# Performance work log

Measured on AMD Instinct MI355X. Metric: run time of the kernel, lower is better.

The kernel has to match this reference:

```python
import jax, jax.numpy as jnp
import numpy as np

IMAGE_SIZE = 256
BATCH = 128
CHANNELS = 3
NUM_STEPS = 32


def dct_matrix(N, dtype=jnp.float32):
    """Orthonormal DCT-II matrix D such that dct(x, norm='ortho') = D @ x."""
    n = jnp.arange(N, dtype=dtype)
    k = n[:, None]
    D = jnp.sqrt(2.0 / N) * jnp.cos(jnp.pi * (n[None, :] + 0.5) * k / N)
    return D.at[0].multiply(1.0 / jnp.sqrt(2.0))


def setup_inputs() -> dict:
    key = jax.random.key(0)
    k1, k2 = jax.random.split(key)
    x = jax.random.normal(k1, (BATCH, CHANNELS, IMAGE_SIZE, IMAGE_SIZE), dtype=jnp.float32)
    # geometric-ish blur schedule sigma in (0, 16]
    blur_sigmas = 0.5 * jnp.arange(1, NUM_STEPS + 1, dtype=jnp.float32)
    fwd_steps = jax.random.randint(k2, (BATCH,), 0, NUM_STEPS)
    return {"x": x, "blur_sigmas": blur_sigmas, "fwd_steps": fwd_steps}


def reference(x, blur_sigmas, fwd_steps):
    N = x.shape[-1]
    D = dct_matrix(N, x.dtype)
    # frequency grid: freqs[k] = pi * k / N
    freqs = jnp.pi * jnp.arange(N, dtype=x.dtype) / N
    freq_sq = freqs[:, None] ** 2 + freqs[None, :] ** 2  # [H, W]
    sigmas = blur_sigmas[fwd_steps][:, None, None, None]  # [B,1,1,1]
    t = sigmas ** 2 / 2.0
    # 2D DCT (ortho): apply D along H and W -> two GEMMs
    coefs = jnp.einsum('hi,bcij,wj->bchw', D, x, D)
    # elementwise spectral heat decay
    coefs = coefs * jnp.exp(-freq_sq * t)
    # 2D inverse DCT (ortho) = transpose transforms
    return jnp.einsum('ih,bchw,jw->bcij', D, coefs, D)
```

## Files before the change

### kernel.cpp

```cpp
#include <hip/hip_runtime.h>
#include <hip/hip_bf16.h>


#define NN 256
#define NSTEP 32

typedef __attribute__((ext_vector_type(8))) __bf16 bf16x8;
typedef __attribute__((ext_vector_type(4))) float f32x4;
typedef __attribute__((ext_vector_type(8))) unsigned short u16x8;
typedef __attribute__((ext_vector_type(4))) unsigned short u16x4;

__device__ __align__(16) float g_D[NN][NN];
__device__ __align__(16) unsigned short g_H[NSTEP][NN][NN];

static __device__ inline unsigned short f2bfu(float x) {
  unsigned u = __builtin_bit_cast(unsigned, x);
  u += 0x7fffu + ((u >> 16) & 1u);
  return (unsigned short)(u >> 16);
}

__global__ void compute_D() {
  int k = blockIdx.x;
  int n = threadIdx.x;
  int q = (k * (2 * n + 1)) & 1023;
  float c = cosf((float)q * (float)(M_PI / 512.0));
  float v = 0.08838834764831845f * c;
  if (k == 0) v *= 0.70710678118654752f;
  g_D[k][n] = v;
}

__global__ void compute_H(const float* __restrict__ sigmas) {
  __shared__ float a[8][NN];
  int s = blockIdx.x >> 5;
  int i0 = (blockIdx.x & 31) * 8;
  int j = threadIdx.x;

  float sg = sigmas[s];
  float t = 0.5f * sg * sg;
  float fk = (float)M_PI * (float)j * (1.0f / (float)NN);
  float m = expf(-fk * fk * t);
#pragma unroll
  for (int r = 0; r < 8; ++r) a[r][j] = g_D[i0 + r][j] * m;
  __syncthreads();

  float acc[8];
#pragma unroll
  for (int r = 0; r < 8; ++r) acc[r] = 0.f;
  for (int k = 0; k < NN; ++k) {
    float d = g_D[k][j];
#pragma unroll
    for (int r = 0; r < 8; ++r) acc[r] += a[r][k] * d;
  }
#pragma unroll
  for (int r = 0; r < 8; ++r) g_H[s][i0 + r][j] = f2bfu(acc[r]);
}

__global__ __launch_bounds__(512, 2) void dct_blur_main(
    const float* __restrict__ x, const int* __restrict__ steps,
    float* __restrict__ out) {
  __shared__ __align__(16) unsigned short Zt[128 * 256];

  int bid = blockIdx.x;
  int img = bid >> 1;
  int half = bid & 1;
  int b = img / 3;
  int s = steps[b];

  const float* X = x + (size_t)img * (NN * NN);
  float* O = out + (size_t)img * (NN * NN);
  const unsigned short* H = &g_H[s][0][0];

  int tid = (int)threadIdx.x;
  int lane = tid & 63;
  int w = tid >> 6;
  int wr = w >> 1;
  int wc = w & 1;
  int l16 = lane & 15;
  int hi = lane >> 4;

  int j0 = half * 128;
  int mrow0 = wr * 64;
  int ncol0 = wc * 64;

  f32x4 acc[4][4];
#pragma unroll
  for (int mi = 0; mi < 4; ++mi)
#pragma unroll
    for (int ni = 0; ni < 4; ++ni)
      acc[mi][ni] = (f32x4){0.f, 0.f, 0.f, 0.f};

#pragma unroll 2
  for (int kk = 0; kk < 8; ++kk) {
    int m0 = kk * 32;
    bf16x8 a[4], bb[4];
#pragma unroll
    for (int mi = 0; mi < 4; ++mi) {
      int row = mrow0 + mi * 16 + l16;
      const f32x4* p = reinterpret_cast<const f32x4*>(X + row * NN + m0 + hi * 8);
      f32x4 v0 = p[0], v1 = p[1];
      u16x8 r;
#pragma unroll
      for (int e = 0; e < 4; ++e) { r[e] = f2bfu(v0[e]); r[4 + e] = f2bfu(v1[e]); }
      a[mi] = __builtin_bit_cast(bf16x8, r);
    }
#pragma unroll
    for (int ni = 0; ni < 4; ++ni) {
      int hrow = j0 + ncol0 + ni * 16 + l16;
      u16x8 g = *reinterpret_cast<const u16x8*>(H + hrow * NN + m0 + hi * 8);
      bb[ni] = __builtin_bit_cast(bf16x8, g);
    }
#pragma unroll
    for (int mi = 0; mi < 4; ++mi)
#pragma unroll
      for (int ni = 0; ni < 4; ++ni)
        acc[mi][ni] = __builtin_amdgcn_mfma_f32_16x16x32_bf16(a[mi], bb[ni], acc[mi][ni], 0, 0, 0);
  }

#pragma unroll
  for (int mi = 0; mi < 4; ++mi) {
#pragma unroll
    for (int ni = 0; ni < 4; ++ni) {
      int j = ncol0 + ni * 16 + l16;
      int kb = mrow0 + mi * 16 + 4 * hi;
      u16x4 pk;
#pragma unroll
      for (int r = 0; r < 4; ++r) pk[r] = f2bfu(acc[mi][ni][r]);
      int idx = ((j << 8) + kb) ^ ((j & 7) << 3);
      *reinterpret_cast<u16x4*>(&Zt[idx]) = pk;
    }
  }

  __syncthreads();

  f32x4 acc2[4][4];
#pragma unroll
  for (int mi = 0; mi < 4; ++mi)
#pragma unroll
    for (int ni = 0; ni < 4; ++ni)
      acc2[mi][ni] = (f32x4){0.f, 0.f, 0.f, 0.f};

#pragma unroll 2
  for (int kk = 0; kk < 8; ++kk) {
    int k0 = kk * 32;
    bf16x8 a2[4], b2[4];
#pragma unroll
    for (int mi = 0; mi < 4; ++mi) {
      int irow = mrow0 + mi * 16 + l16;
      u16x8 g = *reinterpret_cast<const u16x8*>(H + irow * NN + k0 + hi * 8);
      a2[mi] = __builtin_bit_cast(bf16x8, g);
    }
#pragma unroll
    for (int ni = 0; ni < 4; ++ni) {
      int jr = ncol0 + ni * 16 + l16;
      int idx = ((jr << 8) + k0 + hi * 8) ^ ((jr & 7) << 3);
      u16x8 z = *reinterpret_cast<const u16x8*>(&Zt[idx]);
      b2[ni] = __builtin_bit_cast(bf16x8, z);
    }
#pragma unroll
    for (int mi = 0; mi < 4; ++mi)
#pragma unroll
      for (int ni = 0; ni < 4; ++ni)
        acc2[mi][ni] = __builtin_amdgcn_mfma_f32_16x16x32_bf16(a2[mi], b2[ni], acc2[mi][ni], 0, 0, 0);
  }

#pragma unroll
  for (int mi = 0; mi < 4; ++mi) {
#pragma unroll
    for (int ni = 0; ni < 4; ++ni) {
      int ibase = mrow0 + mi * 16 + 4 * hi;
      int jg = j0 + ncol0 + ni * 16 + l16;
#pragma unroll
      for (int r = 0; r < 4; ++r)
        O[(ibase + r) * NN + jg] = acc2[mi][ni][r];
    }
  }
}

extern "C" void kernel_launch(void* const* d_in, const int* in_sizes, int n_in,
                              void* d_out, int out_size, void* d_ws, size_t ws_size,
                              hipStream_t stream) {
  (void)in_sizes; (void)n_in; (void)out_size; (void)d_ws; (void)ws_size;
  const float* x = (const float*)d_in[0];
  const float* sigmas = (const float*)d_in[1];
  const int* steps = (const int*)d_in[2];
  float* out = (float*)d_out;

  compute_D<<<dim3(NN), dim3(NN), 0, stream>>>();
  compute_H<<<dim3(NSTEP * 32), dim3(NN), 0, stream>>>(sigmas);
  dct_blur_main<<<dim3(768), dim3(512), 0, stream>>>(x, steps, out);
}
```

Baseline: 282.2 us.

## Build H via trig-sum closed form and split main GEMMs into two global passes

The precompute is replaced: instead of building the DCT matrix and doing a 256^3 matmul per step, H is derived from per-step cosine/sine sums (compute_U) using a recurrence for the Gaussian weights, then assembled elementwise. The fused main kernel is split into two kernels that pass the intermediate bf16 product through a global scratch buffer, using 256-thread blocks over image quadrants with an XCD-aware block remap. This is meant to cut precompute cost and raise occupancy, at the price of an extra global round-trip for the intermediate and reduced precision in the H construction.

```diff
diff --git a/kernel.cpp b/kernel.cpp
--- a/kernel.cpp
+++ b/kernel.cpp
@@ -1,17 +1,22 @@
 #include <hip/hip_runtime.h>
 #include <hip/hip_bf16.h>
+#include <math.h>
 
 
 #define NN 256
 #define NSTEP 32
+#define NIMG 384
 
 typedef __attribute__((ext_vector_type(8))) __bf16 bf16x8;
+typedef __attribute__((ext_vector_type(4))) __bf16 bf16x4;
 typedef __attribute__((ext_vector_type(4))) float f32x4;
 typedef __attribute__((ext_vector_type(8))) unsigned short u16x8;
 typedef __attribute__((ext_vector_type(4))) unsigned short u16x4;
 
-__device__ __align__(16) float g_D[NN][NN];
+__device__ __align__(16) float g_Uc[NSTEP][512];
+__device__ __align__(16) float g_Us[NSTEP][512];
 __device__ __align__(16) unsigned short g_H[NSTEP][NN][NN];
+__device__ __align__(16) unsigned short g_PT[NIMG * NN * NN];
 
 static __device__ inline unsigned short f2bfu(float x) {
   unsigned u = __builtin_bit_cast(unsigned, x);
@@ -19,68 +24,66 @@
   return (unsigned short)(u >> 16);
 }
 
-__global__ void compute_D() {
-  int k = blockIdx.x;
-  int n = threadIdx.x;
-  int q = (k * (2 * n + 1)) & 1023;
-  float c = cosf((float)q * (float)(M_PI / 512.0));
-  float v = 0.08838834764831845f * c;
-  if (k == 0) v *= 0.70710678118654752f;
-  g_D[k][n] = v;
-}
-
-__global__ void compute_H(const float* __restrict__ sigmas) {
-  __shared__ float a[8][NN];
-  int s = blockIdx.x >> 5;
-  int i0 = (blockIdx.x & 31) * 8;
-  int j = threadIdx.x;
-
+__global__ void compute_U(const float* __restrict__ sigmas) {
+  int s = blockIdx.x >> 3;
+  int q = ((blockIdx.x & 7) << 6) + threadIdx.x;
+  int p = 2 * q + 1;
   float sg = sigmas[s];
   float t = 0.5f * sg * sg;
-  float fk = (float)M_PI * (float)j * (1.0f / (float)NN);
-  float m = expf(-fk * fk * t);
-#pragma unroll
-  for (int r = 0; r < 8; ++r) a[r][j] = g_D[i0 + r][j] * m;
-  __syncthreads();
-
-  float acc[8];
-#pragma unroll
-  for (int r = 0; r < 8; ++r) acc[r] = 0.f;
-  for (int k = 0; k < NN; ++k) {
-    float d = g_D[k][j];
-#pragma unroll
-    for (int r = 0; r < 8; ++r) acc[r] += a[r][k] * d;
-  }
-#pragma unroll
-  for (int r = 0; r < 8; ++r) g_H[s][i0 + r][j] = f2bfu(acc[r]);
-}
-
-__global__ __launch_bounds__(512, 2) void dct_blur_main(
-    const float* __restrict__ x, const int* __restrict__ steps,
-    float* __restrict__ out) {
-  __shared__ __align__(16) unsigned short Zt[128 * 256];
-
+  float c = (float)(M_PI / 256.0) * (float)(M_PI / 256.0) * t;
+  float m = __expf(-c);
+  float ratio = __expf(-3.0f * c);
+  float qf = __expf(-2.0f * c);
+  float sumc = 0.70710678118654752f;
+  float sums = 0.0f;
+  for (int k = 1; k < NN; ++k) {
+    int ph = (k * p) & 1023;
+    float ang = (float)ph * (float)(M_PI / 512.0);
+    float sn, cs;
+    sincosf(ang, &sn, &cs);
+    sumc += m * cs;
+    sums += m * sn;
+    m *= ratio;
+    ratio *= qf;
+  }
+  g_Uc[s][q] = sumc;
+  g_Us[s][q] = sums;
+}
+
+__global__ void compute_H(const float* __restrict__ sigmas) {
+  int s = blockIdx.x >> 8;
+  int i = blockIdx.x & 255;
+  int j = threadIdx.x;
+  int q1 = ((2 * (i - j) - 1) & 1023) >> 1;
+  int q2 = ((2 * (i + j) + 1) & 1023) >> 1;
+  float phi = (float)i * (float)(M_PI / 512.0);
+  float sp, cp;
+  sincosf(phi, &sp, &cp);
+  float v = (g_Uc[s][q1] + g_Uc[s][q2]) * cp - (g_Us[s][q1] + g_Us[s][q2]) * sp;
+  v *= (1.0f / (float)NN);
+  if (i == 0) v *= 0.70710678118654752f;
+  g_H[s][i][j] = f2bfu(v);
+}
+
+__global__ __launch_bounds__(256, 3) void dct_pass1(
+    const float* __restrict__ x, const int* __restrict__ steps) {
   int bid = blockIdx.x;
-  int img = bid >> 1;
-  int half = bid & 1;
-  int b = img / 3;
-  int s = steps[b];
+  int task = (bid & 7) * 192 + (bid >> 3);
+  int img = task >> 2;
+  int quad = task & 3;
+  int s = steps[img / 3];
 
   const float* X = x + (size_t)img * (NN * NN);
-  float* O = out + (size_t)img * (NN * NN);
   const unsigned short* H = &g_H[s][0][0];
+  unsigned short* PT = g_PT + (size_t)img * (NN * NN);
 
   int tid = (int)threadIdx.x;
   int lane = tid & 63;
   int w = tid >> 6;
-  int wr = w >> 1;
-  int wc = w & 1;
   int l16 = lane & 15;
   int hi = lane >> 4;
-
-  int j0 = half * 128;
-  int mrow0 = wr * 64;
-  int ncol0 = wc * 64;
+  int mrow0 = (quad >> 1) * 128 + (w >> 1) * 64;
+  int ncol0 = (quad & 1) * 128 + (w & 1) * 64;
 
   f32x4 acc[4][4];
 #pragma unroll
@@ -94,20 +97,20 @@
     int m0 = kk * 32;
     bf16x8 a[4], bb[4];
 #pragma unroll
+    for (int ni = 0; ni < 4; ++ni) {
+      int hrow = ncol0 + ni * 16 + l16;
+      u16x8 g = *reinterpret_cast<const u16x8*>(H + hrow * NN + m0 + hi * 8);
+      bb[ni] = __builtin_bit_cast(bf16x8, g);
+    }
+#pragma unroll
     for (int mi = 0; mi < 4; ++mi) {
       int row = mrow0 + mi * 16 + l16;
       const f32x4* p = reinterpret_cast<const f32x4*>(X + row * NN + m0 + hi * 8);
       f32x4 v0 = p[0], v1 = p[1];
-      u16x8 r;
-#pragma unroll
-      for (int e = 0; e < 4; ++e) { r[e] = f2bfu(v0[e]); r[4 + e] = f2bfu(v1[e]); }
-      a[mi] = __builtin_bit_cast(bf16x8, r);
-    }
-#pragma unroll
-    for (int ni = 0; ni < 4; ++ni) {
-      int hrow = j0 + ncol0 + ni * 16 + l16;
-      u16x8 g = *reinterpret_cast<const u16x8*>(H + hrow * NN + m0 + hi * 8);
-      bb[ni] = __builtin_bit_cast(bf16x8, g);
+      bf16x8 av;
+#pragma unroll
+      for (int e = 0; e < 4; ++e) { av[e] = (__bf16)v0[e]; av[4 + e] = (__bf16)v1[e]; }
+      a[mi] = av;
     }
 #pragma unroll
     for (int mi = 0; mi < 4; ++mi)
@@ -121,46 +124,63 @@
 #pragma unroll
     for (int ni = 0; ni < 4; ++ni) {
       int j = ncol0 + ni * 16 + l16;
-      int kb = mrow0 + mi * 16 + 4 * hi;
-      u16x4 pk;
-#pragma unroll
-      for (int r = 0; r < 4; ++r) pk[r] = f2bfu(acc[mi][ni][r]);
-      int idx = ((j << 8) + kb) ^ ((j & 7) << 3);
-      *reinterpret_cast<u16x4*>(&Zt[idx]) = pk;
-    }
-  }
-
-  __syncthreads();
-
-  f32x4 acc2[4][4];
+      int rb = mrow0 + mi * 16 + 4 * hi;
+      bf16x4 pk;
+#pragma unroll
+      for (int r = 0; r < 4; ++r) pk[r] = (__bf16)acc[mi][ni][r];
+      *reinterpret_cast<u16x4*>(PT + j * NN + rb) = __builtin_bit_cast(u16x4, pk);
+    }
+  }
+}
+
+__global__ __launch_bounds__(256, 3) void dct_pass2(
+    const int* __restrict__ steps, float* __restrict__ out) {
+  int bid = blockIdx.x;
+  int task = (bid & 7) * 192 + (bid >> 3);
+  int img = task >> 2;
+  int quad = task & 3;
+  int s = steps[img / 3];
+
+  const unsigned short* H = &g_H[s][0][0];
+  const unsigned short* PT = g_PT + (size_t)img * (NN * NN);
+  float* O = out + (size_t)img * (NN * NN);
+
+  int tid = (int)threadIdx.x;
+  int lane = tid & 63;
+  int w = tid >> 6;
+  int l16 = lane & 15;
+  int hi = lane >> 4;
+  int mrow0 = (quad >> 1) * 128 + (w >> 1) * 64;
+  int ncol0 = (quad & 1) * 128 + (w & 1) * 64;
+
+  f32x4 acc[4][4];
 #pragma unroll
   for (int mi = 0; mi < 4; ++mi)
 #pragma unroll
     for (int ni = 0; ni < 4; ++ni)
-      acc2[mi][ni] = (f32x4){0.f, 0.f, 0.f, 0.f};
+      acc[mi][ni] = (f32x4){0.f, 0.f, 0.f, 0.f};
 
 #pragma unroll 2
   for (int kk = 0; kk < 8; ++kk) {
     int k0 = kk * 32;
-    bf16x8 a2[4], b2[4];
+    bf16x8 a[4], bb[4];
 #pragma unroll
     for (int mi = 0; mi < 4; ++mi) {
       int irow = mrow0 + mi * 16 + l16;
       u16x8 g = *reinterpret_cast<const u16x8*>(H + irow * NN + k0 + hi * 8);
-      a2[mi] = __builtin_bit_cast(bf16x8, g);
-    }
-#pragma unroll
-    for (int ni = 0; ni < 4; ++ni) {
-      int jr = ncol0 + ni * 16 + l16;
-      int idx = ((jr << 8) + k0 + hi * 8) ^ ((jr & 7) << 3);
-      u16x8 z = *reinterpret_cast<const u16x8*>(&Zt[idx]);
-      b2[ni] = __builtin_bit_cast(bf16x8, z);
+      a[mi] = __builtin_bit_cast(bf16x8, g);
+    }
+#pragma unroll
+    for (int ni = 0; ni < 4; ++ni) {
+      int jrow = ncol0 + ni * 16 + l16;
+      u16x8 z = *reinterpret_cast<const u16x8*>(PT + jrow * NN + k0 + hi * 8);
+      bb[ni] = __builtin_bit_cast(bf16x8, z);
     }
 #pragma unroll
     for (int mi = 0; mi < 4; ++mi)
 #pragma unroll
       for (int ni = 0; ni < 4; ++ni)
-        acc2[mi][ni] = __builtin_amdgcn_mfma_f32_16x16x32_bf16(a2[mi], b2[ni], acc2[mi][ni], 0, 0, 0);
+        acc[mi][ni] = __builtin_amdgcn_mfma_f32_16x16x32_bf16(a[mi], bb[ni], acc[mi][ni], 0, 0, 0);
   }
 
 #pragma unroll
@@ -168,10 +188,10 @@
 #pragma unroll
     for (int ni = 0; ni < 4; ++ni) {
       int ibase = mrow0 + mi * 16 + 4 * hi;
-      int jg = j0 + ncol0 + ni * 16 + l16;
+      int jg = ncol0 + ni * 16 + l16;
 #pragma unroll
       for (int r = 0; r < 4; ++r)
-        O[(ibase + r) * NN + jg] = acc2[mi][ni][r];
+        O[(ibase + r) * NN + jg] = acc[mi][ni][r];
     }
   }
 }
@@ -185,7 +205,8 @@
   const int* steps = (const int*)d_in[2];
   float* out = (float*)d_out;
 
-  compute_D<<<dim3(NN), dim3(NN), 0, stream>>>();
-  compute_H<<<dim3(NSTEP * 32), dim3(NN), 0, stream>>>(sigmas);
-  dct_blur_main<<<dim3(768), dim3(512), 0, stream>>>(x, steps, out);
-}
+  compute_U<<<dim3(NSTEP * 8), dim3(64), 0, stream>>>(sigmas);
+  compute_H<<<dim3(NSTEP * NN), dim3(NN), 0, stream>>>(sigmas);
+  dct_pass1<<<dim3(NIMG * 4), dim3(256), 0, stream>>>(x, steps);
+  dct_pass2<<<dim3(NIMG * 4), dim3(256), 0, stream>>>(steps, out);
+}
```

Result: slower. 332.3 us (+17.7%).
